# Optimization experiments

Measured on AMD Instinct MI355X. Metric: run time of the kernel, lower is better.

## Reference

```python
import jax, jax.numpy as jnp
import numpy as np

N_NODES = 50000
N_EDGES = 800000
IN_DIM = 256
HIDDEN = 32
HEADS = 4
OUT_DIM = 2
NEG_SLOPE = 0.2  # PyG GATConv default LeakyReLU slope


def setup_inputs() -> dict:
    key = jax.random.key(0)
    ks = jax.random.split(key, 12)
    s = 0.05
    return {
        "x": jax.random.normal(ks[0], (N_NODES, IN_DIM), dtype=jnp.float32),
        "edge_index": jax.random.randint(ks[1], (2, N_EDGES), 0, N_NODES, dtype=jnp.int32),
        # conv1: in_dim -> hidden, heads=4, concat
        "W1": jax.random.normal(ks[2], (IN_DIM, HEADS * HIDDEN), dtype=jnp.float32) * s,
        "att_src1": jax.random.normal(ks[3], (HEADS, HIDDEN), dtype=jnp.float32) * s,
        "att_dst1": jax.random.normal(ks[4], (HEADS, HIDDEN), dtype=jnp.float32) * s,
        "b1": jnp.zeros((HEADS * HIDDEN,), dtype=jnp.float32),
        # conv2: heads*hidden -> hidden, heads=1, mean (concat=False)
        "W2": jax.random.normal(ks[5], (HEADS * HIDDEN, 1 * HIDDEN), dtype=jnp.float32) * s,
        "att_src2": jax.random.normal(ks[6], (1, HIDDEN), dtype=jnp.float32) * s,
        "att_dst2": jax.random.normal(ks[7], (1, HIDDEN), dtype=jnp.float32) * s,
        "b2": jnp.zeros((HIDDEN,), dtype=jnp.float32),
        # final classifier
        "lin_w": jax.random.normal(ks[8], (HIDDEN, OUT_DIM), dtype=jnp.float32) * s,
        "lin_b": jnp.zeros((OUT_DIM,), dtype=jnp.float32),
    }


def gat_conv(x, src, dst, W, att_src, att_dst, bias, concat):
    """PyG-style GATConv (v1), eval mode (no dropout), self-loops already in src/dst."""
    N = x.shape[0]
    H, C = att_src.shape
    h = (x @ W).reshape(N, H, C)                       # [N,H,C]
    a_s = jnp.sum(h * att_src, axis=-1)                # [N,H]
    a_d = jnp.sum(h * att_dst, axis=-1)                # [N,H]
    e = jax.nn.leaky_relu(a_s[src] + a_d[dst], NEG_SLOPE)  # [E,H]
    # numerically-stable softmax over edges grouped by destination node
    m = jax.ops.segment_max(e, dst, num_segments=N)    # [N,H]
    p = jnp.exp(e - m[dst])
    denom = jax.ops.segment_sum(p, dst, num_segments=N)
    alpha = p / denom[dst]                             # [E,H]
    out = jax.ops.segment_sum(alpha[:, :, None] * h[src], dst, num_segments=N)  # [N,H,C]
    out = out.reshape(N, H * C) if concat else out.mean(axis=1)
    return out + bias


def reference(x, edge_index, W1, att_src1, att_dst1, b1, W2, att_src2, att_dst2, b2, lin_w, lin_b):
    N = x.shape[0]
    loops = jnp.arange(N, dtype=edge_index.dtype)      # PyG default add_self_loops=True
    src = jnp.concatenate([edge_index[0], loops])
    dst = jnp.concatenate([edge_index[1], loops])
    h = jax.nn.elu(gat_conv(x, src, dst, W1, att_src1, att_dst1, b1, concat=True))
    h = jax.nn.elu(gat_conv(h, src, dst, W2, att_src2, att_dst2, b2, concat=False))
    return h @ lin_w + lin_b
```

## Files before the change

kernel.cpp:

```cpp
#include <hip/hip_runtime.h>
#include <hip/hip_fp16.h>

#define IN_DIM 256
#define HID 32
#define HEADS 4
#define F1 128
#define BSHIFT 9
#define MAXBUK 128

static __device__ __forceinline__ float leaky(float x){ return x > 0.f ? x : 0.2f*x; }
static __device__ __forceinline__ float elu(float x){ return x > 0.f ? x : (__expf(x) - 1.f); }

static __device__ __forceinline__ unsigned short f2bf(float f){
  unsigned int u = __float_as_uint(f);
  u += 0x7FFFu + ((u >> 16) & 1u);
  return (unsigned short)(u >> 16);
}
static __device__ __forceinline__ float bf2f(unsigned short h){
  return __uint_as_float(((unsigned int)h) << 16);
}
static __device__ __forceinline__ unsigned int pack2(unsigned short a, unsigned short b){
  return (unsigned int)a | ((unsigned int)b << 16);
}
static __device__ __forceinline__ unsigned short f2h(float f){
  return __half_as_ushort(__float2half(f));
}
static __device__ __forceinline__ float hlo(unsigned int u){
  return __half2float(__ushort_as_half((unsigned short)(u & 0xFFFFu)));
}
static __device__ __forceinline__ float hhi(unsigned int u){
  return __half2float(__ushort_as_half((unsigned short)(u >> 16)));
}

__device__ __forceinline__ int block_excl_scan(int v, int tid, int* total){
  __shared__ int ws[8];
  int lane = tid & 63, w = tid >> 6;
  int incl = v;
  #pragma unroll
  for (int d = 1; d < 64; d <<= 1){ int o = __shfl_up(incl, d); if (lane >= d) incl += o; }
  if (lane == 63) ws[w] = incl;
  __syncthreads();
  if (tid == 0){ int s = 0; for (int i = 0; i < 4; ++i){ int t = ws[i]; ws[i] = s; s += t; } ws[4] = s; }
  __syncthreads();
  *total = ws[4];
  int e = ws[w] + incl - v;
  __syncthreads();
  return e;
}

__global__ __launch_bounds__(256) void bukcnt_kernel(const int* __restrict__ dsts,
    int* __restrict__ cnt_blk, const float* __restrict__ W1,
    unsigned short* __restrict__ Wh, unsigned short* __restrict__ Wl,
    int E, int nbuk, int stride){
  __shared__ int lcnt[MAXBUK];
  int tid = threadIdx.x, blk = blockIdx.x;
  int gid = blk*256 + tid;
  if (gid < IN_DIM*F1){
    int n = gid >> 8, k = gid & 255;
    float w = W1[(size_t)k*F1 + n];
    unsigned short h = f2bf(w);
    Wh[gid] = h;
    Wl[gid] = f2bf(w - bf2f(h));
  }
  if (tid < nbuk) lcnt[tid] = 0;
  __syncthreads();
  int base = blk*2048;
  #pragma unroll
  for (int j = 0; j < 8; ++j){
    int i = base + tid + j*256;
    if (i < E) atomicAdd(&lcnt[dsts[i] >> BSHIFT], 1);
  }
  __syncthreads();
  if (tid < nbuk) cnt_blk[tid*stride + blk] = lcnt[tid];
}

__global__ __launch_bounds__(256) void bukscan1_kernel(int* __restrict__ cnt_blk,
    int* __restrict__ btot, int nchk, int stride){
  int b = blockIdx.x, tid = threadIdx.x;
  int carry = 0;
  for (int s = 0; s < nchk; s += 256){
    int i = s + tid;
    int v = (i < nchk) ? cnt_blk[b*stride + i] : 0;
    int tot; int e = block_excl_scan(v, tid, &tot);
    if (i < nchk) cnt_blk[b*stride + i] = carry + e;
    carry += tot;
  }
  if (tid == 0) btot[b] = carry;
}

__global__ __launch_bounds__(256) void bukscan2_kernel(const int* __restrict__ btot,
    int* __restrict__ bucket_base, int* __restrict__ offs, int nbuk, int Nn, int E){
  int tid = threadIdx.x;
  int v = (tid < nbuk) ? btot[tid] : 0;
  int tot; int e = block_excl_scan(v, tid, &tot);
  if (tid <= nbuk) bucket_base[tid] = e;
  if (tid == 0) offs[Nn] = E;
}

__global__ __launch_bounds__(256) void bukscat_kernel(const int* __restrict__ srcs,
    const int* __restrict__ dsts, const int* __restrict__ cnt_blk,
    const int* __restrict__ bucket_base, unsigned int* __restrict__ im,
    int E, int nbuk, int stride){
  __shared__ int lcur[MAXBUK];
  int tid = threadIdx.x, blk = blockIdx.x;
  if (tid < nbuk) lcur[tid] = bucket_base[tid] + cnt_blk[tid*stride + blk];
  __syncthreads();
  int base = blk*2048;
  #pragma unroll
  for (int j = 0; j < 8; ++j){
    int i = base + tid + j*256;
    if (i < E){
      int s = srcs[i], d = dsts[i];
      int r = atomicAdd(&lcur[d >> BSHIFT], 1);
      im[r] = (unsigned)s | (((unsigned)d & 511u) << 16);
    }
  }
}

__global__ __launch_bounds__(256) void bukfine_kernel(const unsigned int* __restrict__ im,
    const int* __restrict__ bucket_base, int* __restrict__ offs, int* __restrict__ csr, int Nn){
  __shared__ int lcnt[512], lpfx[512];
  int b = blockIdx.x, tid = threadIdx.x;
  int node0 = b << BSHIFT;
  int nn = min(512, Nn - node0);
  lcnt[tid] = 0; lcnt[tid+256] = 0;
  __syncthreads();
  int ebeg = bucket_base[b], eend = bucket_base[b+1];
  for (int i = ebeg + tid; i < eend; i += 256)
    atomicAdd(&lcnt[im[i] >> 16], 1);
  __syncthreads();
  int carry = 0;
  for (int s = 0; s < 512; s += 256){
    int v = lcnt[s + tid];
    int tot; int e = block_excl_scan(v, tid, &tot);
    lpfx[s + tid] = carry + e;
    carry += tot;
  }
  __syncthreads();
  if (tid < nn) offs[node0 + tid] = ebeg + lpfx[tid];
  if (tid + 256 < nn) offs[node0 + tid + 256] = ebeg + lpfx[tid + 256];
  lcnt[tid] = ebeg + lpfx[tid];
  lcnt[tid+256] = ebeg + lpfx[tid+256];
  __syncthreads();
  for (int i = ebeg + tid; i < eend; i += 256){
    unsigned int u = im[i];
    int pos = atomicAdd(&lcnt[u >> 16], 1);
    csr[pos] = (int)(u & 0xFFFFu);
  }
}

typedef __attribute__((ext_vector_type(8))) short bf8_t;
typedef __attribute__((ext_vector_type(4))) float f4_t;
typedef _Float16 f16x8 __attribute__((ext_vector_type(8)));

__global__ __launch_bounds__(256) void gemm1_kernel(const float* __restrict__ x,
    const unsigned short* __restrict__ Wh, const unsigned short* __restrict__ Wl,
    const float* __restrict__ att_src, const float* __restrict__ att_dst,
    unsigned short* __restrict__ h1b, float* __restrict__ as1, float* __restrict__ ad1, int M){
  __shared__ uint4 AhV[64][5], AlV[64][5];
  __shared__ uint4 BhV[128][5], BlV[128][5];
  const int tid = threadIdx.x;
  const int m0 = blockIdx.x*64;
  const int wave = tid >> 6, lane = tid & 63;
  const int quad = lane >> 4, l16 = lane & 15;
  const int wr = (wave & 1)*32;
  const int wc = (wave >> 1)*64;
  f4_t acc[2][4];
  #pragma unroll
  for (int r = 0; r < 2; ++r)
    #pragma unroll
    for (int c = 0; c < 4; ++c)
      #pragma unroll
      for (int i = 0; i < 4; ++i) acc[r][c][i] = 0.f;

  const int ar = tid >> 2, akc = tid & 3;
  const bool aok = (m0 + ar) < M;
  const float* ap = x + (size_t)(m0 + ar)*IN_DIM + 8*akc;
  const int bn = tid >> 1, bkc = (tid & 1)*2;
  const unsigned short* bph = Wh + (size_t)bn*256 + 16*(tid & 1);
  const unsigned short* bpl = Wl + (size_t)bn*256 + 16*(tid & 1);

  for (int k0 = 0; k0 < IN_DIM; k0 += 32){
    float4 a0 = make_float4(0.f,0.f,0.f,0.f), a1 = a0;
    if (aok){ a0 = *(const float4*)(ap + k0); a1 = *(const float4*)(ap + k0 + 4); }
    float v[8] = {a0.x,a0.y,a0.z,a0.w,a1.x,a1.y,a1.z,a1.w};
    unsigned short hh[8], ll[8];
    #pragma unroll
    for (int j = 0; j < 8; ++j){
      unsigned short h = f2bf(v[j]); hh[j] = h; ll[j] = f2bf(v[j] - bf2f(h));
    }
    uint4 hv; hv.x = pack2(hh[0],hh[1]); hv.y = pack2(hh[2],hh[3]); hv.z = pack2(hh[4],hh[5]); hv.w = pack2(hh[6],hh[7]);
    uint4 lv; lv.x = pack2(ll[0],ll[1]); lv.y = pack2(ll[2],ll[3]); lv.z = pack2(ll[4],ll[5]); lv.w = pack2(ll[6],ll[7]);
    AhV[ar][akc] = hv;
    AlV[ar][akc] = lv;
    BhV[bn][bkc+0] = *(const uint4*)(bph + k0);
    BhV[bn][bkc+1] = *(const uint4*)(bph + k0 + 8);
    BlV[bn][bkc+0] = *(const uint4*)(bpl + k0);
    BlV[bn][bkc+1] = *(const uint4*)(bpl + k0 + 8);
    __syncthreads();

    bf8_t arh[2], arl[2], brh[4], brl[4];
    #pragma unroll
    for (int r = 0; r < 2; ++r){
      arh[r] = *(const bf8_t*)&AhV[wr + r*16 + l16][quad];
      arl[r] = *(const bf8_t*)&AlV[wr + r*16 + l16][quad];
    }
    #pragma unroll
    for (int c = 0; c < 4; ++c){
      brh[c] = *(const bf8_t*)&BhV[wc + c*16 + l16][quad];
      brl[c] = *(const bf8_t*)&BlV[wc + c*16 + l16][quad];
    }
    #pragma unroll
    for (int r = 0; r < 2; ++r)
      #pragma unroll
      for (int c = 0; c < 4; ++c){
        acc[r][c] = __builtin_amdgcn_mfma_f32_16x16x32_bf16(arh[r], brh[c], acc[r][c], 0, 0, 0);
        acc[r][c] = __builtin_amdgcn_mfma_f32_16x16x32_bf16(arh[r], brl[c], acc[r][c], 0, 0, 0);
        acc[r][c] = __builtin_amdgcn_mfma_f32_16x16x32_bf16(arl[r], brh[c], acc[r][c], 0, 0, 0);
      }
    __syncthreads();
  }

  const int head0 = wc >> 5;
  float sv[4], dv[4];
  #pragma unroll
  for (int c = 0; c < 4; ++c){
    int col_in_head = (c & 1)*16 + l16;
    sv[c] = att_src[(head0 + (c >> 1))*HID + col_in_head];
    dv[c] = att_dst[(head0 + (c >> 1))*HID + col_in_head];
  }
  #pragma unroll
  for (int r = 0; r < 2; ++r){
    #pragma unroll
    for (int i = 0; i < 4; ++i){
      int row = m0 + wr + r*16 + quad*4 + i;
      bool ok = row < M;
      float hv0 = acc[r][0][i], hv1 = acc[r][1][i], hv2 = acc[r][2][i], hv3 = acc[r][3][i];
      if (ok){
        unsigned short* hp = h1b + (size_t)row*F1 + wc + l16;
        hp[0]  = f2h(hv0); hp[16] = f2h(hv1); hp[32] = f2h(hv2); hp[48] = f2h(hv3);
      }
      float p0 = hv0*sv[0] + hv1*sv[1];
      float p1 = hv2*sv[2] + hv3*sv[3];
      float q0 = hv0*dv[0] + hv1*dv[1];
      float q1 = hv2*dv[2] + hv3*dv[3];
      p0 += __shfl_xor(p0,1); p0 += __shfl_xor(p0,2); p0 += __shfl_xor(p0,4); p0 += __shfl_xor(p0,8);
      p1 += __shfl_xor(p1,1); p1 += __shfl_xor(p1,2); p1 += __shfl_xor(p1,4); p1 += __shfl_xor(p1,8);
      q0 += __shfl_xor(q0,1); q0 += __shfl_xor(q0,2); q0 += __shfl_xor(q0,4); q0 += __shfl_xor(q0,8);
      q1 += __shfl_xor(q1,1); q1 += __shfl_xor(q1,2); q1 += __shfl_xor(q1,4); q1 += __shfl_xor(q1,8);
      if (ok && l16 == 0){
        as1[row*4 + head0]     = p0;
        as1[row*4 + head0 + 1] = p1;
        ad1[row*4 + head0]     = q0;
        ad1[row*4 + head0 + 1] = q1;
      }
    }
  }
}

__global__ __launch_bounds__(256) void agg1_kernel(const unsigned int* __restrict__ h1b,
    const float* __restrict__ a_s1, const float* __restrict__ a_d1,
    const int* __restrict__ offs, const int* __restrict__ csr,
    const float* __restrict__ b1, uint4* __restrict__ h1a4, int N){
  int n = blockIdx.x*4 + (threadIdx.x >> 6);
  if (n >= N) return;
  const int lane = threadIdx.x & 63;
  const int sub  = lane >> 4;
  const int cl   = lane & 15;
  const int head = cl >> 2;
  const int j    = cl & 3;
  const int pbase = (lane & ~15) + (head << 2);
  const float ad = a_d1[n*4+head];
  const int cw = 4*cl;
  float a0=0,a1=0,a2=0,a3=0,a4=0,a5=0,a6=0,a7=0,den=0;
  if (sub == 0){
    float p = __expf(leaky(a_s1[n*4+head] + ad));
    uint4 u = *(const uint4*)(h1b + (size_t)n*64 + cw);
    a0 = p*hlo(u.x); a1 = p*hhi(u.x); a2 = p*hlo(u.y); a3 = p*hhi(u.y);
    a4 = p*hlo(u.z); a5 = p*hhi(u.z); a6 = p*hlo(u.w); a7 = p*hhi(u.w);
    den = p;
  }
  const int beg = offs[n], end = offs[n+1];
  int e = beg + sub;
  for (; e + 12 < end; e += 16){
    int s0 = csr[e], s1 = csr[e+4], s2 = csr[e+8], s3 = csr[e+12];
    int sown = j == 0 ? s0 : (j == 1 ? s1 : (j == 2 ? s2 : s3));
    float pown = __expf(leaky(a_s1[sown*4+head] + ad));
    float p0 = __shfl(pown, pbase+0);
    float p1 = __shfl(pown, pbase+1);
    float p2 = __shfl(pown, pbase+2);
    float p3 = __shfl(pown, pbase+3);
    uint4 u0 = *(const uint4*)(h1b + (size_t)s0*64 + cw);
    uint4 u1 = *(const uint4*)(h1b + (size_t)s1*64 + cw);
    uint4 u2 = *(const uint4*)(h1b + (size_t)s2*64 + cw);
    uint4 u3 = *(const uint4*)(h1b + (size_t)s3*64 + cw);
    a0 += p0*hlo(u0.x) + p1*hlo(u1.x) + p2*hlo(u2.x) + p3*hlo(u3.x);
    a1 += p0*hhi(u0.x) + p1*hhi(u1.x) + p2*hhi(u2.x) + p3*hhi(u3.x);
    a2 += p0*hlo(u0.y) + p1*hlo(u1.y) + p2*hlo(u2.y) + p3*hlo(u3.y);
    a3 += p0*hhi(u0.y) + p1*hhi(u1.y) + p2*hhi(u2.y) + p3*hhi(u3.y);
    a4 += p0*hlo(u0.z) + p1*hlo(u1.z) + p2*hlo(u2.z) + p3*hlo(u3.z);
    a5 += p0*hhi(u0.z) + p1*hhi(u1.z) + p2*hhi(u2.z) + p3*hhi(u3.z);
    a6 += p0*hlo(u0.w) + p1*hlo(u1.w) + p2*hlo(u2.w) + p3*hlo(u3.w);
    a7 += p0*hhi(u0.w) + p1*hhi(u1.w) + p2*hhi(u2.w) + p3*hhi(u3.w);
    den += p0 + p1 + p2 + p3;
  }
  for (; e < end; e += 4){
    int s = csr[e];
    float p = __expf(leaky(a_s1[s*4+head] + ad));
    uint4 u = *(const uint4*)(h1b + (size_t)s*64 + cw);
    a0 += p*hlo(u.x); a1 += p*hhi(u.x); a2 += p*hlo(u.y); a3 += p*hhi(u.y);
    a4 += p*hlo(u.z); a5 += p*hhi(u.z); a6 += p*hlo(u.w); a7 += p*hhi(u.w);
    den += p;
  }
  #pragma unroll
  for (int off = 16; off < 64; off <<= 1){
    a0 += __shfl_xor(a0,off); a1 += __shfl_xor(a1,off);
    a2 += __shfl_xor(a2,off); a3 += __shfl_xor(a3,off);
    a4 += __shfl_xor(a4,off); a5 += __shfl_xor(a5,off);
    a6 += __shfl_xor(a6,off); a7 += __shfl_xor(a7,off);
    den += __shfl_xor(den,off);
  }
  if (sub == 0){
    float inv = 1.f/den;
    int ch = 8*cl;
    float4 b0 = *(const float4*)(b1 + ch);
    float4 b4 = *(const float4*)(b1 + ch + 4);
    uint4 w;
    w.x = pack2(f2h(elu(a0*inv+b0.x)), f2h(elu(a1*inv+b0.y)));
    w.y = pack2(f2h(elu(a2*inv+b0.z)), f2h(elu(a3*inv+b0.w)));
    w.z = pack2(f2h(elu(a4*inv+b4.x)), f2h(elu(a5*inv+b4.y)));
    w.w = pack2(f2h(elu(a6*inv+b4.z)), f2h(elu(a7*inv+b4.w)));
    h1a4[(size_t)n*16 + cl] = w;
  }
}

__global__ __launch_bounds__(256) void gemm2_kernel(const uint4* __restrict__ h1a4, const float* __restrict__ W2,
    const float* __restrict__ att_src, const float* __restrict__ att_dst,
    unsigned short* __restrict__ h2s, float* __restrict__ as2, float* __restrict__ ad2, int M){
  __shared__ unsigned short Ab[64*136];
  __shared__ unsigned short Bh[32*136];
  __shared__ unsigned short Bl[32*136];
  const int tid = threadIdx.x;
  const int m0 = blockIdx.x*64;
  const int wave = tid >> 6, lane = tid & 63;
  const int quad = lane >> 4, l16 = lane & 15;

  #pragma unroll
  for (int p = 0; p < 4; ++p){
    int idx = tid + 256*p;
    int r = idx >> 4, q = idx & 15;
    int row = m0 + r;
    uint4 u = make_uint4(0,0,0,0);
    if (row < M) u = h1a4[(size_t)row*16 + q];
    *(uint4*)&Ab[r*136 + 8*q] = u;
  }
  {
    const float4* w4 = (const float4*)W2;
    #pragma unroll
    for (int p = 0; p < 4; ++p){
      int idx = tid*4 + p;
      float4 v = w4[idx];
      int e0 = idx*4;
      float vv[4] = {v.x, v.y, v.z, v.w};
      #pragma unroll
      for (int t = 0; t < 4; ++t){
        int e = e0 + t, k = e >> 5, n = e & 31;
        __half hi = __float2half(vv[t]);
        __half lo = __float2half((vv[t] - __half2float(hi)) * 4096.f);
        Bh[n*136 + k] = __half_as_ushort(hi);
        Bl[n*136 + k] = __half_as_ushort(lo);
      }
    }
  }
  __syncthreads();

  f4_t acch[2], accl[2];
  #pragma unroll
  for (int c = 0; c < 2; ++c)
    #pragma unroll
    for (int i = 0; i < 4; ++i){ acch[c][i] = 0.f; accl[c][i] = 0.f; }

  #pragma unroll
  for (int kc = 0; kc < 4; ++kc){
    f16x8 a = *(const f16x8*)&Ab[(16*wave + l16)*136 + kc*32 + quad*8];
    #pragma unroll
    for (int c = 0; c < 2; ++c){
      f16x8 bh = *(const f16x8*)&Bh[(16*c + l16)*136 + kc*32 + quad*8];
      f16x8 bl = *(const f16x8*)&Bl[(16*c + l16)*136 + kc*32 + quad*8];
      acch[c] = __builtin_amdgcn_mfma_f32_16x16x32_f16(a, bh, acch[c], 0, 0, 0);
      accl[c] = __builtin_amdgcn_mfma_f32_16x16x32_f16(a, bl, accl[c], 0, 0, 0);
    }
  }

  const float sv0 = att_src[l16],      dv0 = att_dst[l16];
  const float sv1 = att_src[l16 + 16], dv1 = att_dst[l16 + 16];
  #pragma unroll
  for (int i = 0; i < 4; ++i){
    int row = m0 + 16*wave + quad*4 + i;
    bool ok = row < M;
    float v0 = acch[0][i] + accl[0][i] * (1.f/4096.f);
    float v1 = acch[1][i] + accl[1][i] * (1.f/4096.f);
    if (ok){
      h2s[(size_t)row*32 + l16]      = f2h(v0);
      h2s[(size_t)row*32 + l16 + 16] = f2h(v1);
    }
    float ps = v0*sv0 + v1*sv1;
    float pd = v0*dv0 + v1*dv1;
    ps += __shfl_xor(ps,1); ps += __shfl_xor(ps,2); ps += __shfl_xor(ps,4); ps += __shfl_xor(ps,8);
    pd += __shfl_xor(pd,1); pd += __shfl_xor(pd,2); pd += __shfl_xor(pd,4); pd += __shfl_xor(pd,8);
    if (ok && l16 == 0){ as2[row] = ps; ad2[row] = pd; }
  }
}

__global__ __launch_bounds__(256) void agg2_kernel(const unsigned int* __restrict__ h2b,
    const float* __restrict__ as2, const float* __restrict__ ad2,
    const int* __restrict__ offs, const int* __restrict__ csr,
    const float* __restrict__ b2, const float* __restrict__ linw, const float* __restrict__ linb,
    float* __restrict__ out, int N){
  int n = blockIdx.x*4 + (threadIdx.x >> 6);
  if (n >= N) return;
  const int lane = threadIdx.x & 63;
  const int sub  = lane >> 3;
  const int cl   = lane & 7;
  const int j    = cl & 3;
  const int pbase = lane & ~7;
  const int cw   = 2*cl;
  const float ad = ad2[n];
  float a0=0,a1=0,a2=0,a3=0,den=0;
  if (sub == 0){
    float p = __expf(leaky(as2[n] + ad));
    uint2 u = *(const uint2*)(h2b + (size_t)n*16 + cw);
    a0 = p*hlo(u.x); a1 = p*hhi(u.x); a2 = p*hlo(u.y); a3 = p*hhi(u.y);
    den = p;
  }
  const int beg = offs[n], end = offs[n+1];
  int e = beg + sub;
  for (; e + 24 < end; e += 32){
    int s0 = csr[e], s1 = csr[e+8], s2 = csr[e+16], s3 = csr[e+24];
    int sown = j == 0 ? s0 : (j == 1 ? s1 : (j == 2 ? s2 : s3));
    float pown = __expf(leaky(as2[sown] + ad));
    float p0 = __shfl(pown, pbase+0);
    float p1 = __shfl(pown, pbase+1);
    float p2 = __shfl(pown, pbase+2);
    float p3 = __shfl(pown, pbase+3);
    uint2 u0 = *(const uint2*)(h2b + (size_t)s0*16 + cw);
    uint2 u1 = *(const uint2*)(h2b + (size_t)s1*16 + cw);
    uint2 u2 = *(const uint2*)(h2b + (size_t)s2*16 + cw);
    uint2 u3 = *(const uint2*)(h2b + (size_t)s3*16 + cw);
    a0 += p0*hlo(u0.x) + p1*hlo(u1.x) + p2*hlo(u2.x) + p3*hlo(u3.x);
    a1 += p0*hhi(u0.x) + p1*hhi(u1.x) + p2*hhi(u2.x) + p3*hhi(u3.x);
    a2 += p0*hlo(u0.y) + p1*hlo(u1.y) + p2*hlo(u2.y) + p3*hlo(u3.y);
    a3 += p0*hhi(u0.y) + p1*hhi(u1.y) + p2*hhi(u2.y) + p3*hhi(u3.y);
    den += p0 + p1 + p2 + p3;
  }
  for (; e < end; e += 8){
    int s = csr[e];
    float p = __expf(leaky(as2[s] + ad));
    uint2 u = *(const uint2*)(h2b + (size_t)s*16 + cw);
    a0 += p*hlo(u.x); a1 += p*hhi(u.x); a2 += p*hlo(u.y); a3 += p*hhi(u.y);
    den += p;
  }
  #pragma unroll
  for (int off = 8; off < 64; off <<= 1){
    a0 += __shfl_xor(a0,off); a1 += __shfl_xor(a1,off);
    a2 += __shfl_xor(a2,off); a3 += __shfl_xor(a3,off);
    den += __shfl_xor(den,off);
  }
  float inv = 1.f/den;
  int ch = 4*cl;
  float o0 = elu(a0*inv + b2[ch+0]);
  float o1 = elu(a1*inv + b2[ch+1]);
  float o2 = elu(a2*inv + b2[ch+2]);
  float o3 = elu(a3*inv + b2[ch+3]);
  float r0 = o0*linw[2*(ch+0)]   + o1*linw[2*(ch+1)]   + o2*linw[2*(ch+2)]   + o3*linw[2*(ch+3)];
  float r1 = o0*linw[2*(ch+0)+1] + o1*linw[2*(ch+1)+1] + o2*linw[2*(ch+2)+1] + o3*linw[2*(ch+3)+1];
  r0 += __shfl_xor(r0,1); r0 += __shfl_xor(r0,2); r0 += __shfl_xor(r0,4);
  r1 += __shfl_xor(r1,1); r1 += __shfl_xor(r1,2); r1 += __shfl_xor(r1,4);
  if (lane == 0){
    out[(size_t)n*2+0] = r0 + linb[0];
    out[(size_t)n*2+1] = r1 + linb[1];
  }
}

extern "C" void kernel_launch(void* const* d_in, const int* in_sizes, int n_in,
                              void* d_out, int out_size, void* d_ws, size_t ws_size,
                              hipStream_t stream) {
  const float* x    = (const float*)d_in[0];
  const int*   ei   = (const int*)  d_in[1];
  const float* W1   = (const float*)d_in[2];
  const float* as1w = (const float*)d_in[3];
  const float* ad1w = (const float*)d_in[4];
  const float* b1   = (const float*)d_in[5];
  const float* W2   = (const float*)d_in[6];
  const float* as2w = (const float*)d_in[7];
  const float* ad2w = (const float*)d_in[8];
  const float* b2   = (const float*)d_in[9];
  const float* linw = (const float*)d_in[10];
  const float* linb = (const float*)d_in[11];
  float* out = (float*)d_out;

  const int N = in_sizes[0] / IN_DIM;
  const int E = in_sizes[1] / 2;

  const int NBUK = (N + 511) >> BSHIFT;
  const int NCHK = (E + 2047) / 2048;
  const int CSTR = (NCHK + 3) & ~3;

  char* ws = (char*)d_ws;
  auto alloc = [&](size_t bytes) -> char* {
    char* p = ws; ws += (bytes + 255) & ~(size_t)255; return p;
  };
  unsigned short* h1b = (unsigned short*)alloc((size_t)N*F1*2);
  uint4* h1a4 = (uint4*)alloc((size_t)N*F1*2);
  unsigned short* h2s = (unsigned short*)alloc((size_t)N*HID*2);
  float* a_s1 = (float*)alloc((size_t)N*4*4);
  float* a_d1 = (float*)alloc((size_t)N*4*4);
  float* a_s2 = (float*)alloc((size_t)N*4);
  float* a_d2 = (float*)alloc((size_t)N*4);
  int* cnt_blk = (int*)alloc((size_t)NBUK*CSTR*4);
  int* btot    = (int*)alloc((size_t)(NBUK+1)*4);
  int* bbase   = (int*)alloc((size_t)(NBUK+1)*4);
  int* offs    = (int*)alloc((size_t)(N+1)*4);
  int* csr     = (int*)alloc((size_t)E*4);
  unsigned int* im = (unsigned int*)alloc((size_t)E*4);
  unsigned short* W1h = (unsigned short*)alloc((size_t)IN_DIM*F1*2);
  unsigned short* W1l = (unsigned short*)alloc((size_t)IN_DIM*F1*2);

  const int* srcs = ei;
  const int* dsts = ei + E;

  bukcnt_kernel<<<NCHK, 256, 0, stream>>>(dsts, cnt_blk, W1, W1h, W1l, E, NBUK, CSTR);
  bukscan1_kernel<<<NBUK, 256, 0, stream>>>(cnt_blk, btot, NCHK, CSTR);
  bukscan2_kernel<<<1, 256, 0, stream>>>(btot, bbase, offs, NBUK, N, E);
  bukscat_kernel<<<NCHK, 256, 0, stream>>>(srcs, dsts, cnt_blk, bbase, im, E, NBUK, CSTR);
  bukfine_kernel<<<NBUK, 256, 0, stream>>>(im, bbase, offs, csr, N);
  gemm1_kernel<<<(N+63)/64, 256, 0, stream>>>(x, W1h, W1l, as1w, ad1w, h1b, a_s1, a_d1, N);
  agg1_kernel<<<(N+3)/4, 256, 0, stream>>>((const unsigned int*)h1b, a_s1, a_d1, offs, csr, b1, h1a4, N);
  gemm2_kernel<<<(N+63)/64, 256, 0, stream>>>(h1a4, W2, as2w, ad2w, h2s, a_s2, a_d2, N);
  agg2_kernel<<<(N+3)/4, 256, 0, stream>>>((const unsigned int*)h2s, a_s2, a_d2, offs, csr, b2, linw, linb, out, N);
}
```

Before: 233.0 us.

## Precompute per-edge attention exponentials in separate edge-parallel kernels

The CSR now packs the destination node into the upper 16 bits of each entry alongside the source. Two new edge-parallel kernels use this to compute exp(leaky(a_s[src]+a_d[dst])) per edge for both layers and store the results in dedicated buffers. The aggregation kernels then read these precomputed weights instead of computing them cooperatively with gathers and wave shuffles. This takes the exp and gather latency off the aggregation inner loop, at the cost of two extra launches and writing and re-reading about 16 MB of per-edge weights.

New measurement: 251.1 us. 1.08x slower.

```diff
diff --git a/kernel.cpp b/kernel.cpp
--- a/kernel.cpp
+++ b/kernel.cpp
@@ -118,7 +118,7 @@
 }
 
 __global__ __launch_bounds__(256) void bukfine_kernel(const unsigned int* __restrict__ im,
-    const int* __restrict__ bucket_base, int* __restrict__ offs, int* __restrict__ csr, int Nn){
+    const int* __restrict__ bucket_base, int* __restrict__ offs, unsigned int* __restrict__ csr, int Nn){
   __shared__ int lcnt[512], lpfx[512];
   int b = blockIdx.x, tid = threadIdx.x;
   int node0 = b << BSHIFT;
@@ -144,9 +144,33 @@
   __syncthreads();
   for (int i = ebeg + tid; i < eend; i += 256){
     unsigned int u = im[i];
-    int pos = atomicAdd(&lcnt[u >> 16], 1);
-    csr[pos] = (int)(u & 0xFFFFu);
-  }
+    int ld = (int)(u >> 16);
+    int pos = atomicAdd(&lcnt[ld], 1);
+    csr[pos] = (u & 0xFFFFu) | ((unsigned)(node0 + ld) << 16);
+  }
+}
+
+__global__ __launch_bounds__(256) void pk1_kernel(const unsigned int* __restrict__ csr,
+    const float* __restrict__ a_s1, const float* __restrict__ a_d1,
+    float4* __restrict__ p1, int E){
+  int e = blockIdx.x*256 + threadIdx.x;
+  if (e >= E) return;
+  unsigned int u = csr[e];
+  int s = (int)(u & 0xFFFFu), d = (int)(u >> 16);
+  float4 as = *(const float4*)(a_s1 + (size_t)s*4);
+  float4 ad = *(const float4*)(a_d1 + (size_t)d*4);
+  p1[e] = make_float4(__expf(leaky(as.x + ad.x)), __expf(leaky(as.y + ad.y)),
+                      __expf(leaky(as.z + ad.z)), __expf(leaky(as.w + ad.w)));
+}
+
+__global__ __launch_bounds__(256) void pk2_kernel(const unsigned int* __restrict__ csr,
+    const float* __restrict__ as2, const float* __restrict__ ad2,
+    float* __restrict__ p2, int E){
+  int e = blockIdx.x*256 + threadIdx.x;
+  if (e >= E) return;
+  unsigned int u = csr[e];
+  int s = (int)(u & 0xFFFFu), d = (int)(u >> 16);
+  p2[e] = __expf(leaky(as2[s] + ad2[d]));
 }
 
 typedef __attribute__((ext_vector_type(8))) short bf8_t;
@@ -260,7 +284,8 @@
 
 __global__ __launch_bounds__(256) void agg1_kernel(const unsigned int* __restrict__ h1b,
     const float* __restrict__ a_s1, const float* __restrict__ a_d1,
-    const int* __restrict__ offs, const int* __restrict__ csr,
+    const float* __restrict__ p1,
+    const int* __restrict__ offs, const unsigned int* __restrict__ csr,
     const float* __restrict__ b1, uint4* __restrict__ h1a4, int N){
   int n = blockIdx.x*4 + (threadIdx.x >> 6);
   if (n >= N) return;
@@ -268,13 +293,10 @@
   const int sub  = lane >> 4;
   const int cl   = lane & 15;
   const int head = cl >> 2;
-  const int j    = cl & 3;
-  const int pbase = (lane & ~15) + (head << 2);
-  const float ad = a_d1[n*4+head];
-  const int cw = 4*cl;
+  const int cw   = 4*cl;
   float a0=0,a1=0,a2=0,a3=0,a4=0,a5=0,a6=0,a7=0,den=0;
   if (sub == 0){
-    float p = __expf(leaky(a_s1[n*4+head] + ad));
+    float p = __expf(leaky(a_s1[n*4+head] + a_d1[n*4+head]));
     uint4 u = *(const uint4*)(h1b + (size_t)n*64 + cw);
     a0 = p*hlo(u.x); a1 = p*hhi(u.x); a2 = p*hlo(u.y); a3 = p*hhi(u.y);
     a4 = p*hlo(u.z); a5 = p*hhi(u.z); a6 = p*hlo(u.w); a7 = p*hhi(u.w);
@@ -283,30 +305,31 @@
   const int beg = offs[n], end = offs[n+1];
   int e = beg + sub;
   for (; e + 12 < end; e += 16){
-    int s0 = csr[e], s1 = csr[e+4], s2 = csr[e+8], s3 = csr[e+12];
-    int sown = j == 0 ? s0 : (j == 1 ? s1 : (j == 2 ? s2 : s3));
-    float pown = __expf(leaky(a_s1[sown*4+head] + ad));
-    float p0 = __shfl(pown, pbase+0);
-    float p1 = __shfl(pown, pbase+1);
-    float p2 = __shfl(pown, pbase+2);
-    float p3 = __shfl(pown, pbase+3);
+    int s0 = (int)(csr[e]    & 0xFFFFu);
+    int s1 = (int)(csr[e+4]  & 0xFFFFu);
+    int s2 = (int)(csr[e+8]  & 0xFFFFu);
+    int s3 = (int)(csr[e+12] & 0xFFFFu);
+    float p0 = p1[(size_t)e*4      + head];
+    float p1v = p1[(size_t)(e+4)*4  + head];
+    float p2v = p1[(size_t)(e+8)*4  + head];
+    float p3v = p1[(size_t)(e+12)*4 + head];
     uint4 u0 = *(const uint4*)(h1b + (size_t)s0*64 + cw);
     uint4 u1 = *(const uint4*)(h1b + (size_t)s1*64 + cw);
     uint4 u2 = *(const uint4*)(h1b + (size_t)s2*64 + cw);
     uint4 u3 = *(const uint4*)(h1b + (size_t)s3*64 + cw);
-    a0 += p0*hlo(u0.x) + p1*hlo(u1.x) + p2*hlo(u2.x) + p3*hlo(u3.x);
-    a1 += p0*hhi(u0.x) + p1*hhi(u1.x) + p2*hhi(u2.x) + p3*hhi(u3.x);
-    a2 += p0*hlo(u0.y) + p1*hlo(u1.y) + p2*hlo(u2.y) + p3*hlo(u3.y);
-    a3 += p0*hhi(u0.y) + p1*hhi(u1.y) + p2*hhi(u2.y) + p3*hhi(u3.y);
-    a4 += p0*hlo(u0.z) + p1*hlo(u1.z) + p2*hlo(u2.z) + p3*hlo(u3.z);
-    a5 += p0*hhi(u0.z) + p1*hhi(u1.z) + p2*hhi(u2.z) + p3*hhi(u3.z);
-    a6 += p0*hlo(u0.w) + p1*hlo(u1.w) + p2*hlo(u2.w) + p3*hlo(u3.w);
-    a7 += p0*hhi(u0.w) + p1*hhi(u1.w) + p2*hhi(u2.w) + p3*hhi(u3.w);
-    den += p0 + p1 + p2 + p3;
+    a0 += p0*hlo(u0.x) + p1v*hlo(u1.x) + p2v*hlo(u2.x) + p3v*hlo(u3.x);
+    a1 += p0*hhi(u0.x) + p1v*hhi(u1.x) + p2v*hhi(u2.x) + p3v*hhi(u3.x);
+    a2 += p0*hlo(u0.y) + p1v*hlo(u1.y) + p2v*hlo(u2.y) + p3v*hlo(u3.y);
+    a3 += p0*hhi(u0.y) + p1v*hhi(u1.y) + p2v*hhi(u2.y) + p3v*hhi(u3.y);
+    a4 += p0*hlo(u0.z) + p1v*hlo(u1.z) + p2v*hlo(u2.z) + p3v*hlo(u3.z);
+    a5 += p0*hhi(u0.z) + p1v*hhi(u1.z) + p2v*hhi(u2.z) + p3v*hhi(u3.z);
+    a6 += p0*hlo(u0.w) + p1v*hlo(u1.w) + p2v*hlo(u2.w) + p3v*hlo(u3.w);
+    a7 += p0*hhi(u0.w) + p1v*hhi(u1.w) + p2v*hhi(u2.w) + p3v*hhi(u3.w);
+    den += p0 + p1v + p2v + p3v;
   }
   for (; e < end; e += 4){
-    int s = csr[e];
-    float p = __expf(leaky(a_s1[s*4+head] + ad));
+    int s = (int)(csr[e] & 0xFFFFu);
+    float p = p1[(size_t)e*4 + head];
     uint4 u = *(const uint4*)(h1b + (size_t)s*64 + cw);
     a0 += p*hlo(u.x); a1 += p*hhi(u.x); a2 += p*hlo(u.y); a3 += p*hhi(u.y);
     a4 += p*hlo(u.z); a5 += p*hhi(u.z); a6 += p*hlo(u.w); a7 += p*hhi(u.w);
@@ -414,7 +437,8 @@
 
 __global__ __launch_bounds__(256) void agg2_kernel(const unsigned int* __restrict__ h2b,
     const float* __restrict__ as2, const float* __restrict__ ad2,
-    const int* __restrict__ offs, const int* __restrict__ csr,
+    const float* __restrict__ p2,
+    const int* __restrict__ offs, const unsigned int* __restrict__ csr,
     const float* __restrict__ b2, const float* __restrict__ linw, const float* __restrict__ linb,
     float* __restrict__ out, int N){
   int n = blockIdx.x*4 + (threadIdx.x >> 6);
@@ -422,13 +446,10 @@
   const int lane = threadIdx.x & 63;
   const int sub  = lane >> 3;
   const int cl   = lane & 7;
-  const int j    = cl & 3;
-  const int pbase = lane & ~7;
   const int cw   = 2*cl;
-  const float ad = ad2[n];
   float a0=0,a1=0,a2=0,a3=0,den=0;
   if (sub == 0){
-    float p = __expf(leaky(as2[n] + ad));
+    float p = __expf(leaky(as2[n] + ad2[n]));
     uint2 u = *(const uint2*)(h2b + (size_t)n*16 + cw);
     a0 = p*hlo(u.x); a1 = p*hhi(u.x); a2 = p*hlo(u.y); a3 = p*hhi(u.y);
     den = p;
@@ -436,26 +457,24 @@
   const int beg = offs[n], end = offs[n+1];
   int e = beg + sub;
   for (; e + 24 < end; e += 32){
-    int s0 = csr[e], s1 = csr[e+8], s2 = csr[e+16], s3 = csr[e+24];
-    int sown = j == 0 ? s0 : (j == 1 ? s1 : (j == 2 ? s2 : s3));
-    float pown = __expf(leaky(as2[sown] + ad));
-    float p0 = __shfl(pown, pbase+0);
-    float p1 = __shfl(pown, pbase+1);
-    float p2 = __shfl(pown, pbase+2);
-    float p3 = __shfl(pown, pbase+3);
+    int s0 = (int)(csr[e]    & 0xFFFFu);
+    int s1 = (int)(csr[e+8]  & 0xFFFFu);
+    int s2 = (int)(csr[e+16] & 0xFFFFu);
+    int s3 = (int)(csr[e+24] & 0xFFFFu);
+    float p0 = p2[e], p1v = p2[e+8], p2v = p2[e+16], p3v = p2[e+24];
     uint2 u0 = *(const uint2*)(h2b + (size_t)s0*16 + cw);
     uint2 u1 = *(const uint2*)(h2b + (size_t)s1*16 + cw);
     uint2 u2 = *(const uint2*)(h2b + (size_t)s2*16 + cw);
     uint2 u3 = *(const uint2*)(h2b + (size_t)s3*16 + cw);
-    a0 += p0*hlo(u0.x) + p1*hlo(u1.x) + p2*hlo(u2.x) + p3*hlo(u3.x);
-    a1 += p0*hhi(u0.x) + p1*hhi(u1.x) + p2*hhi(u2.x) + p3*hhi(u3.x);
-    a2 += p0*hlo(u0.y) + p1*hlo(u1.y) + p2*hlo(u2.y) + p3*hlo(u3.y);
-    a3 += p0*hhi(u0.y) + p1*hhi(u1.y) + p2*hhi(u2.y) + p3*hhi(u3.y);
-    den += p0 + p1 + p2 + p3;
+    a0 += p0*hlo(u0.x) + p1v*hlo(u1.x) + p2v*hlo(u2.x) + p3v*hlo(u3.x);
+    a1 += p0*hhi(u0.x) + p1v*hhi(u1.x) + p2v*hhi(u2.x) + p3v*hhi(u3.x);
+    a2 += p0*hlo(u0.y) + p1v*hlo(u1.y) + p2v*hlo(u2.y) + p3v*hlo(u3.y);
+    a3 += p0*hhi(u0.y) + p1v*hhi(u1.y) + p2v*hhi(u2.y) + p3v*hhi(u3.y);
+    den += p0 + p1v + p2v + p3v;
   }
   for (; e < end; e += 8){
-    int s = csr[e];
-    float p = __expf(leaky(as2[s] + ad));
+    int s = (int)(csr[e] & 0xFFFFu);
+    float p = p2[e];
     uint2 u = *(const uint2*)(h2b + (size_t)s*16 + cw);
     a0 += p*hlo(u.x); a1 += p*hhi(u.x); a2 += p*hlo(u.y); a3 += p*hhi(u.y);
     den += p;
@@ -521,13 +540,16 @@
   int* btot    = (int*)alloc((size_t)(NBUK+1)*4);
   int* bbase   = (int*)alloc((size_t)(NBUK+1)*4);
   int* offs    = (int*)alloc((size_t)(N+1)*4);
-  int* csr     = (int*)alloc((size_t)E*4);
-  unsigned int* im = (unsigned int*)alloc((size_t)E*4);
+  unsigned int* csr = (unsigned int*)alloc((size_t)E*4);
+  unsigned int* im  = (unsigned int*)alloc((size_t)E*4);
   unsigned short* W1h = (unsigned short*)alloc((size_t)IN_DIM*F1*2);
   unsigned short* W1l = (unsigned short*)alloc((size_t)IN_DIM*F1*2);
+  float4* p1 = (float4*)alloc((size_t)E*16);
+  float*  p2 = (float*)alloc((size_t)E*4);
 
   const int* srcs = ei;
   const int* dsts = ei + E;
+  const int EB = (E + 255)/256;
 
   bukcnt_kernel<<<NCHK, 256, 0, stream>>>(dsts, cnt_blk, W1, W1h, W1l, E, NBUK, CSTR);
   bukscan1_kernel<<<NBUK, 256, 0, stream>>>(cnt_blk, btot, NCHK, CSTR);
@@ -535,7 +557,9 @@
   bukscat_kernel<<<NCHK, 256, 0, stream>>>(srcs, dsts, cnt_blk, bbase, im, E, NBUK, CSTR);
   bukfine_kernel<<<NBUK, 256, 0, stream>>>(im, bbase, offs, csr, N);
   gemm1_kernel<<<(N+63)/64, 256, 0, stream>>>(x, W1h, W1l, as1w, ad1w, h1b, a_s1, a_d1, N);
-  agg1_kernel<<<(N+3)/4, 256, 0, stream>>>((const unsigned int*)h1b, a_s1, a_d1, offs, csr, b1, h1a4, N);
+  pk1_kernel<<<EB, 256, 0, stream>>>(csr, a_s1, a_d1, p1, E);
+  agg1_kernel<<<(N+3)/4, 256, 0, stream>>>((const unsigned int*)h1b, a_s1, a_d1, (const float*)p1, offs, csr, b1, h1a4, N);
   gemm2_kernel<<<(N+63)/64, 256, 0, stream>>>(h1a4, W2, as2w, ad2w, h2s, a_s2, a_d2, N);
-  agg2_kernel<<<(N+3)/4, 256, 0, stream>>>((const unsigned int*)h2s, a_s2, a_d2, offs, csr, b2, linw, linb, out, N);
-}
+  pk2_kernel<<<EB, 256, 0, stream>>>(csr, a_s2, a_d2, p2, E);
+  agg2_kernel<<<(N+3)/4, 256, 0, stream>>>((const unsigned int*)h2s, a_s2, a_d2, p2, offs, csr, b2, linw, linb, out, N);
+}
```
